# Kernel tuning notes

Measured on AMD Instinct MI355X. Metric: run time of the kernel, lower is better.

Reference implementation:

```python
import jax, jax.numpy as jnp
import numpy as np

L, B, T, E, NH, HD, HID, V = 8, 2, 2048, 1024, 16, 64, 2816, 32000


def _rmsnorm(x, w, eps=1e-6):
    return w * (x * jax.lax.rsqrt(jnp.mean(x * x, axis=-1, keepdims=True) + eps))


def _rope(x, cos, sin):
    # x: [B,H,T,D]; cos/sin: [1,1,T,D/2]
    x1, x2 = jnp.split(x, 2, axis=-1)
    return jnp.concatenate([x1 * cos - x2 * sin, x1 * sin + x2 * cos], axis=-1)


def setup_inputs() -> dict:
    key = jax.random.key(0)
    ks = jax.random.split(key, 7)
    s = 0.02
    return {
        "idx": jax.random.randint(ks[0], (B, T), 0, V),
        "tok_emb": jax.random.normal(ks[1], (V, E), dtype=jnp.float32) * s,
        "qkv_w": jax.random.normal(ks[2], (L, 3 * E, E), dtype=jnp.float32) * s,
        "proj_w": jax.random.normal(ks[3], (L, E, E), dtype=jnp.float32) * s,
        "w1": jax.random.normal(ks[4], (L, HID, E), dtype=jnp.float32) * s,
        "w2": jax.random.normal(ks[5], (L, HID, E), dtype=jnp.float32) * s,
        "w3": jax.random.normal(ks[6], (L, E, HID), dtype=jnp.float32) * s,
        "norm1_w": jnp.ones((L, E), dtype=jnp.float32),
        "norm2_w": jnp.ones((L, E), dtype=jnp.float32),
        "norm_f_w": jnp.ones((E,), dtype=jnp.float32),
    }


def reference(idx, tok_emb, qkv_w, proj_w, w1, w2, w3, norm1_w, norm2_w, norm_f_w):
    x = tok_emb[idx]  # [B,T,E]
    # RoPE cache (start_pos=0, no kv cache -> prefill path)
    half = HD // 2
    inv_freq = 1.0 / (10000.0 ** (jnp.arange(half, dtype=jnp.float32) / half))
    pos = jnp.arange(T, dtype=jnp.float32)
    freqs = pos[:, None] * inv_freq[None, :]  # [T, D/2]
    cos = jnp.cos(freqs)[None, None]
    sin = jnp.sin(freqs)[None, None]
    causal = jnp.tril(jnp.ones((T, T), dtype=bool))
    scale = 1.0 / np.sqrt(HD).astype(np.float32)

    for l in range(L):
        # attention block
        h = _rmsnorm(x, norm1_w[l])
        qkv = h @ qkv_w[l].T  # [B,T,3E]
        q, k, v = jnp.split(qkv, 3, axis=-1)
        q = q.reshape(B, T, NH, HD).transpose(0, 2, 1, 3)
        k = k.reshape(B, T, NH, HD).transpose(0, 2, 1, 3)
        v = v.reshape(B, T, NH, HD).transpose(0, 2, 1, 3)
        q = _rope(q, cos, sin)
        k = _rope(k, cos, sin)
        att = jnp.einsum('bhqd,bhkd->bhqk', q, k) * scale
        att = jnp.where(causal, att, -jnp.inf)
        att = jax.nn.softmax(att, axis=-1)
        o = jnp.einsum('bhqk,bhkd->bhqd', att, v)
        o = o.transpose(0, 2, 1, 3).reshape(B, T, E)
        x = x + o @ proj_w[l].T
        # SwiGLU MLP
        h = _rmsnorm(x, norm2_w[l])
        x = x + (jax.nn.silu(h @ w1[l].T) * (h @ w2[l].T)) @ w3[l].T

    x = _rmsnorm(x, norm_f_w)
    logits = x @ tok_emb.T  # tied lm_head
    return logits
```

## Files before the change

### kernel.cpp

```cpp
#include <hip/hip_runtime.h>

#define GLOBAL_AS __attribute__((address_space(1)))
#define LDS_AS __attribute__((address_space(3)))

typedef unsigned short u16;
typedef unsigned int u32;
typedef __attribute__((ext_vector_type(4))) float f32x4;
typedef __attribute__((ext_vector_type(8))) short bf16x8;

#define TT 2048
#define EE 1024
#define NHH 16
#define HDD 64
#define HIDD 2816
#define VV 32000
#define MM 4096

__device__ __forceinline__ u16 f2bf(float f) {
  u32 u = __builtin_bit_cast(u32, f);
  u += 0x7fffu + ((u >> 16) & 1u);
  return (u16)(u >> 16);
}
__device__ __forceinline__ float bf2f(u16 v) {
  return __builtin_bit_cast(float, (u32)v << 16);
}


__global__ __launch_bounds__(256) void castbf_k(const float* __restrict__ in,
                                                u16* __restrict__ o, long n4) {
  const long i = (long)blockIdx.x * 256 + threadIdx.x;
  if (i >= n4) return;
  const float4 v = ((const float4*)in)[i];
  ((uint2*)o)[i] = make_uint2((u32)f2bf(v.x) | ((u32)f2bf(v.y) << 16),
                              (u32)f2bf(v.z) | ((u32)f2bf(v.w) << 16));
}

__global__ void ropetab_k(float* __restrict__ cosT, float* __restrict__ sinT) {
  const int t = blockIdx.x, j = threadIdx.x;
  const float inv = powf(10000.0f, -(float)j * (1.0f / 32.0f));
  const float f = (float)t * inv;
  cosT[t * 32 + j] = cosf(f);
  sinT[t * 32 + j] = sinf(f);
}

__global__ __launch_bounds__(256) void embed_k(const int* __restrict__ idx,
                                               const float* __restrict__ temb,
                                               float* __restrict__ x) {
  const int row = blockIdx.x;
  const int id = idx[row];
  ((float4*)(x + (size_t)row * EE))[threadIdx.x] =
      ((const float4*)(temb + (size_t)id * EE))[threadIdx.x];
}

__global__ __launch_bounds__(256) void rmsnorm_k(const float* __restrict__ x,
                                                 const float* __restrict__ w,
                                                 u16* __restrict__ o) {
  __shared__ float red[4];
  const int row = blockIdx.x, tid = threadIdx.x;
  const float4 v = ((const float4*)(x + (size_t)row * EE))[tid];
  float ss = v.x * v.x + v.y * v.y + v.z * v.z + v.w * v.w;
#pragma unroll
  for (int off = 32; off; off >>= 1) ss += __shfl_xor(ss, off, 64);
  if ((tid & 63) == 0) red[tid >> 6] = ss;
  __syncthreads();
  const float inv = rsqrtf((red[0] + red[1] + red[2] + red[3]) * (1.0f / 1024.0f) + 1e-6f);
  const float4 wv = ((const float4*)w)[tid];
  const u32 lo = (u32)f2bf(v.x * inv * wv.x) | ((u32)f2bf(v.y * inv * wv.y) << 16);
  const u32 hi = (u32)f2bf(v.z * inv * wv.z) | ((u32)f2bf(v.w * inv * wv.w) << 16);
  ((uint2*)(o + (size_t)row * EE))[tid] = make_uint2(lo, hi);
}

__global__ __launch_bounds__(512) void split_rope_k(const u16* __restrict__ qkv,
                                                    const float* __restrict__ cosT,
                                                    const float* __restrict__ sinT,
                                                    u16* __restrict__ Q, u16* __restrict__ Kc,
                                                    u16* __restrict__ Vt) {
  const int row = blockIdx.x;
  const int b = row >> 11, t = row & 2047;
  const int h = threadIdx.x >> 5, j = threadIdx.x & 31;
  const u16* base = qkv + (size_t)row * (3 * EE);
  const float c = cosT[t * 32 + j], s = sinT[t * 32 + j];
  const float q1 = bf2f(base[h * 64 + j]), q2 = bf2f(base[h * 64 + j + 32]);
  const float k1 = bf2f(base[EE + h * 64 + j]), k2 = bf2f(base[EE + h * 64 + j + 32]);
  const float v1 = bf2f(base[2 * EE + h * 64 + j]), v2 = bf2f(base[2 * EE + h * 64 + j + 32]);
  const size_t bh = (size_t)(b * NHH + h);
  Q[(bh * TT + t) * HDD + j] = f2bf(q1 * c - q2 * s);
  Q[(bh * TT + t) * HDD + j + 32] = f2bf(q1 * s + q2 * c);
  Kc[(bh * TT + t) * HDD + j] = f2bf(k1 * c - k2 * s);
  Kc[(bh * TT + t) * HDD + j + 32] = f2bf(k1 * s + k2 * c);
  Vt[(bh * HDD + j) * TT + t] = f2bf(v1);
  Vt[(bh * HDD + j + 32) * TT + t] = f2bf(v2);
}

template <int OUTBF>
__global__ __launch_bounds__(512, 2) void gemm256p(const u16* __restrict__ A,
                                                   const u16* __restrict__ Bw,
                                                   float* __restrict__ C,
                                                   u16* __restrict__ C16,
                                                   const u16* __restrict__ G,
                                                   int N, int K) {
  __shared__ u16 lds[2 * 32768];
  const int t = threadIdx.x;
  const int lane = t & 63;
  const int wid = t >> 6;
  const int wr = wid >> 2;
  const int wc = wid & 3;
  const int l15 = lane & 15, lg = lane >> 4;
  const int bid = blockIdx.x;
  const int row0 = (bid & 15) << 8;
  const int col0 = (bid >> 4) << 8;
  const int NT = K >> 6;

  const int sr = t >> 3;
  const int su8 = (((t & 7) ^ (sr & 7)) << 3);
  const int t8 = t << 3;
  const u16* aG[4];
#pragma unroll
  for (int ga = 0; ga < 4; ++ga)
    aG[ga] = A + (size_t)(row0 + ga * 64 + sr) * K + su8;
  const u16* bG[4];
#pragma unroll
  for (int gb = 0; gb < 4; ++gb) {
    const int q = (gb * 2 + (sr >> 5)) & 3;
    const int nh = gb >> 1;
    bG[gb] = Bw + (size_t)(col0 + q * 64 + nh * 32 + (sr & 31)) * K + su8;
  }

  const int u0 = ((lg ^ (l15 & 7)) << 3);
  const int u1 = (((4 | lg) ^ (l15 & 7)) << 3);
  const int arow = (wr * 128 + l15) << 6;
  const int brow = 16384 + ((wc * 32 + l15) << 6);

  f32x4 acc[8][4] = {};

#define STA(nb, ga, k0n)                                                              \
  __builtin_amdgcn_global_load_lds((const GLOBAL_AS void*)(aG[ga] + (k0n)),           \
                                   (LDS_AS void*)((nb) + (ga)*4096 + t8), 16, 0, 0)
#define STB(nb, gb, k0n)                                                              \
  __builtin_amdgcn_global_load_lds((const GLOBAL_AS void*)(bG[gb] + (k0n)),           \
                                   (LDS_AS void*)((nb) + 16384 + (gb)*4096 + t8), 16, 0, 0)

  {
    u16* nb = lds;
    STA(nb, 0, 0); STA(nb, 2, 0);
    STB(nb, 0, 0); STB(nb, 1, 0);
    STB(nb, 2, 0); STB(nb, 3, 0);
    STA(nb, 1, 0); STA(nb, 3, 0);
  }

  bf16x8 af[4][2], bl[2][2], bh[2][2];

  for (int kt = 0; kt < NT; ++kt) {
    const bool st = (kt + 1 < NT);
    const int k0n = (kt + 1) << 6;
    const u16* cb = lds + (kt & 1) * 32768;
    u16* nb = lds + ((kt + 1) & 1) * 32768;

    asm volatile("s_waitcnt vmcnt(4)" ::: "memory");
    __builtin_amdgcn_s_barrier();
#pragma unroll
    for (int mi = 0; mi < 4; ++mi) {
      af[mi][0] = *(const bf16x8*)&cb[arow + mi * 1024 + u0];
      af[mi][1] = *(const bf16x8*)&cb[arow + mi * 1024 + u1];
    }
#pragma unroll
    for (int ni = 0; ni < 2; ++ni) {
      bl[ni][0] = *(const bf16x8*)&cb[brow + ni * 1024 + u0];
      bl[ni][1] = *(const bf16x8*)&cb[brow + ni * 1024 + u1];
    }
    if (st) { STA(nb, 0, k0n); STA(nb, 2, k0n); }
    __builtin_amdgcn_s_setprio(1);
#pragma unroll
    for (int mi = 0; mi < 4; ++mi)
#pragma unroll
      for (int ni = 0; ni < 2; ++ni) {
        acc[mi][ni] = __builtin_amdgcn_mfma_f32_16x16x32_bf16(af[mi][0], bl[ni][0], acc[mi][ni], 0, 0, 0);
        acc[mi][ni] = __builtin_amdgcn_mfma_f32_16x16x32_bf16(af[mi][1], bl[ni][1], acc[mi][ni], 0, 0, 0);
      }
    __builtin_amdgcn_s_setprio(0);

    if (st) { asm volatile("s_waitcnt vmcnt(4)" ::: "memory"); }
    else    { asm volatile("s_waitcnt vmcnt(2)" ::: "memory"); }
    __builtin_amdgcn_s_barrier();
#pragma unroll
    for (int ni = 0; ni < 2; ++ni) {
      bh[ni][0] = *(const bf16x8*)&cb[brow + 8192 + ni * 1024 + u0];
      bh[ni][1] = *(const bf16x8*)&cb[brow + 8192 + ni * 1024 + u1];
    }
    if (st) { STB(nb, 0, k0n); STB(nb, 1, k0n); }
    __builtin_amdgcn_s_setprio(1);
#pragma unroll
    for (int mi = 0; mi < 4; ++mi)
#pragma unroll
      for (int ni = 0; ni < 2; ++ni) {
        acc[mi][2 + ni] = __builtin_amdgcn_mfma_f32_16x16x32_bf16(af[mi][0], bh[ni][0], acc[mi][2 + ni], 0, 0, 0);
        acc[mi][2 + ni] = __builtin_amdgcn_mfma_f32_16x16x32_bf16(af[mi][1], bh[ni][1], acc[mi][2 + ni], 0, 0, 0);
      }
    __builtin_amdgcn_s_setprio(0);

    if (st) { asm volatile("s_waitcnt vmcnt(4)" ::: "memory"); }
    else    { asm volatile("s_waitcnt vmcnt(0)" ::: "memory"); }
    __builtin_amdgcn_s_barrier();
#pragma unroll
    for (int mi = 0; mi < 4; ++mi) {
      af[mi][0] = *(const bf16x8*)&cb[arow + (4 + mi) * 1024 + u0];
      af[mi][1] = *(const bf16x8*)&cb[arow + (4 + mi) * 1024 + u1];
    }
    if (st) { STB(nb, 2, k0n); STB(nb, 3, k0n); }
    __builtin_amdgcn_s_setprio(1);
#pragma unroll
    for (int mi = 0; mi < 4; ++mi)
#pragma unroll
      for (int ni = 0; ni < 2; ++ni) {
        acc[4 + mi][2 + ni] = __builtin_amdgcn_mfma_f32_16x16x32_bf16(af[mi][0], bh[ni][0], acc[4 + mi][2 + ni], 0, 0, 0);
        acc[4 + mi][2 + ni] = __builtin_amdgcn_mfma_f32_16x16x32_bf16(af[mi][1], bh[ni][1], acc[4 + mi][2 + ni], 0, 0, 0);
      }
    __builtin_amdgcn_s_setprio(0);

    if (st) { STA(nb, 1, k0n); STA(nb, 3, k0n); }
    __builtin_amdgcn_s_setprio(1);
#pragma unroll
    for (int mi = 0; mi < 4; ++mi)
#pragma unroll
      for (int ni = 0; ni < 2; ++ni) {
        acc[4 + mi][ni] = __builtin_amdgcn_mfma_f32_16x16x32_bf16(af[mi][0], bl[ni][0], acc[4 + mi][ni], 0, 0, 0);
        acc[4 + mi][ni] = __builtin_amdgcn_mfma_f32_16x16x32_bf16(af[mi][1], bl[ni][1], acc[4 + mi][ni], 0, 0, 0);
      }
    __builtin_amdgcn_s_setprio(0);
  }
#undef STA
#undef STB

#pragma unroll
  for (int m = 0; m < 8; ++m) {
    const int row = row0 + wr * 128 + m * 16 + lg * 4;
#pragma unroll
    for (int n = 0; n < 4; ++n) {
      const int col = col0 + wc * 64 + n * 16 + l15;
#pragma unroll
      for (int r = 0; r < 4; ++r) {
        const size_t o = (size_t)(row + r) * N + col;
        if (OUTBF == 0) {
          C[o] = acc[m][n][r];
        } else if (OUTBF == 1) {
          C16[o] = f2bf(acc[m][n][r]);
        } else {
          const float g = bf2f(G[o]);
          C16[o] = f2bf(g / (1.0f + __expf(-g)) * acc[m][n][r]);
        }
      }
    }
  }
}

__global__ __launch_bounds__(256, 2) void gemm128r(const u16* __restrict__ A,
                                                   const u16* __restrict__ Bw,
                                                   float* __restrict__ C,
                                                   const float* __restrict__ R,
                                                   int N, int K) {
  __shared__ u16 lds[4 * 8192];
  const int t = threadIdx.x;
  const int lane = t & 63;
  const int wid = t >> 6;
  const int wr = wid >> 1;
  const int wc = wid & 1;
  const int l15 = lane & 15, lg = lane >> 4;
  const int bid = blockIdx.x;
  const int row0 = (bid & 31) << 7;
  const int col0 = (bid >> 5) << 7;
  const int NT = K >> 5;

  const int rA = t >> 2;
  const int usw = (((t & 3) ^ ((t >> 3) & 3)) << 3);
  const u16* sA0 = A + (size_t)(row0 + rA) * K + usw;
  const u16* sA1 = A + (size_t)(row0 + 64 + rA) * K + usw;
  const u16* sB0 = Bw + (size_t)(col0 + rA) * K + usw;
  const u16* sB1 = Bw + (size_t)(col0 + 64 + rA) * K + usw;
  const int dst = t << 3;

  const int e8 = ((lg ^ ((l15 >> 1) & 3)) << 3);
  const int aoff = (wr * 64 + l15) * 32 + e8;
  const int boff = 4096 + (wc * 64 + l15) * 32 + e8;

  f32x4 acc[4][4] = {};

  auto stage = [&](int kt) {
    u16* base = &lds[(kt & 3) * 8192];
    const size_t ko = (size_t)kt * 32;
    __builtin_amdgcn_global_load_lds((const GLOBAL_AS void*)(sA0 + ko),
                                     (LDS_AS void*)(base + dst), 16, 0, 0);
    __builtin_amdgcn_global_load_lds((const GLOBAL_AS void*)(sA1 + ko),
                                     (LDS_AS void*)(base + 2048 + dst), 16, 0, 0);
    __builtin_amdgcn_global_load_lds((const GLOBAL_AS void*)(sB0 + ko),
                                     (LDS_AS void*)(base + 4096 + dst), 16, 0, 0);
    __builtin_amdgcn_global_load_lds((const GLOBAL_AS void*)(sB1 + ko),
                                     (LDS_AS void*)(base + 6144 + dst), 16, 0, 0);
  };

  stage(0);
  stage(1);
  stage(2);

  for (int kt = 0; kt < NT; ++kt) {
    const int rem = NT - 1 - kt;
    if (rem >= 2) {
      asm volatile("s_waitcnt vmcnt(8)" ::: "memory");
    } else if (rem == 1) {
      asm volatile("s_waitcnt vmcnt(4)" ::: "memory");
    } else {
      asm volatile("s_waitcnt vmcnt(0)" ::: "memory");
    }
    __builtin_amdgcn_s_barrier();
    if (kt + 3 < NT) stage(kt + 3);
    const u16* base = &lds[(kt & 3) * 8192];
    bf16x8 af[4], bfv[4];
#pragma unroll
    for (int m = 0; m < 4; ++m) af[m] = *(const bf16x8*)&base[aoff + m * 512];
#pragma unroll
    for (int n = 0; n < 4; ++n) bfv[n] = *(const bf16x8*)&base[boff + n * 512];
    __builtin_amdgcn_s_setprio(1);
#pragma unroll
    for (int m = 0; m < 4; ++m)
#pragma unroll
      for (int n = 0; n < 4; ++n)
        acc[m][n] = __builtin_amdgcn_mfma_f32_16x16x32_bf16(af[m], bfv[n], acc[m][n], 0, 0, 0);
    __builtin_amdgcn_s_setprio(0);
  }

#pragma unroll
  for (int m = 0; m < 4; ++m) {
    const int row = row0 + wr * 64 + m * 16 + lg * 4;
#pragma unroll
    for (int n = 0; n < 4; ++n) {
      const int col = col0 + wc * 64 + n * 16 + l15;
#pragma unroll
      for (int r = 0; r < 4; ++r) {
        const size_t o = (size_t)(row + r) * N + col;
        C[o] = acc[m][n][r] + R[o];
      }
    }
  }
}

__global__ __launch_bounds__(256) void attn_k(const u16* __restrict__ Q,
                                              const u16* __restrict__ Kc,
                                              const u16* __restrict__ Vt,
                                              u16* __restrict__ O) {
  __shared__ u16 P_lds[4][32][72];
  const int bh = blockIdx.y;
  const int q0 = blockIdx.x * 128;
  const int lane = threadIdx.x & 63;
  const int w = threadIdx.x >> 6;
  const int l15 = lane & 15, lg = lane >> 4;
  const int qbase = q0 + w * 32;

  bf16x8 qf[2][2];
#pragma unroll
  for (int am = 0; am < 2; ++am)
#pragma unroll
    for (int ks = 0; ks < 2; ++ks)
      qf[am][ks] = *(const bf16x8*)&Q[((size_t)bh * TT + qbase + am * 16 + l15) * HDD + ks * 32 + lg * 8];

  bf16x8 ones;
#pragma unroll
  for (int i = 0; i < 8; ++i) ones[i] = (short)0x3F80;

  f32x4 oacc[2][4] = {};
  f32x4 lacc[2] = {};

  const int ntile = (q0 + 128) >> 6;
  for (int kt = 0; kt < ntile; ++kt) {
    const int k0 = kt << 6;
    f32x4 s[2][4];
    bf16x8 kf0[4], kf1[4];
#pragma unroll
    for (int an = 0; an < 4; ++an) {
      kf0[an] = *(const bf16x8*)&Kc[((size_t)bh * TT + k0 + an * 16 + l15) * HDD + lg * 8];
      kf1[an] = *(const bf16x8*)&Kc[((size_t)bh * TT + k0 + an * 16 + l15) * HDD + 32 + lg * 8];
    }
    __builtin_amdgcn_s_setprio(1);
#pragma unroll
    for (int an = 0; an < 4; ++an) {
#pragma unroll
      for (int am = 0; am < 2; ++am) {
        f32x4 z = {0.0f, 0.0f, 0.0f, 0.0f};
        z = __builtin_amdgcn_mfma_f32_16x16x32_bf16(qf[am][0], kf0[an], z, 0, 0, 0);
        s[am][an] = __builtin_amdgcn_mfma_f32_16x16x32_bf16(qf[am][1], kf1[an], z, 0, 0, 0);
      }
    }
    __builtin_amdgcn_s_setprio(0);
    const bool diag = (k0 + 64) > q0;
#pragma unroll
    for (int am = 0; am < 2; ++am)
#pragma unroll
      for (int an = 0; an < 4; ++an)
#pragma unroll
        for (int r = 0; r < 4; ++r) {
          float v = s[am][an][r] * 0.125f;
          if (diag) {
            const int qrow = qbase + am * 16 + lg * 4 + r;
            const int kcol = k0 + an * 16 + l15;
            if (kcol > qrow) v = -1e30f;
          }
          s[am][an][r] = __expf(v);
        }
#pragma unroll
    for (int am = 0; am < 2; ++am)
#pragma unroll
      for (int an = 0; an < 4; ++an)
#pragma unroll
        for (int r = 0; r < 4; ++r)
          P_lds[w][am * 16 + lg * 4 + r][an * 16 + l15] = f2bf(s[am][an][r]);
#pragma unroll
    for (int ks = 0; ks < 2; ++ks) {
      bf16x8 pf[2];
#pragma unroll
      for (int am = 0; am < 2; ++am)
        pf[am] = *(const bf16x8*)&P_lds[w][am * 16 + l15][ks * 32 + lg * 8];
      __builtin_amdgcn_s_setprio(1);
#pragma unroll
      for (int dn = 0; dn < 4; ++dn) {
        const bf16x8 vf = *(const bf16x8*)&Vt[((size_t)bh * HDD + dn * 16 + l15) * TT + k0 + ks * 32 + lg * 8];
#pragma unroll
        for (int am = 0; am < 2; ++am)
          oacc[am][dn] = __builtin_amdgcn_mfma_f32_16x16x32_bf16(pf[am], vf, oacc[am][dn], 0, 0, 0);
      }
#pragma unroll
      for (int am = 0; am < 2; ++am)
        lacc[am] = __builtin_amdgcn_mfma_f32_16x16x32_bf16(pf[am], ones, lacc[am], 0, 0, 0);
      __builtin_amdgcn_s_setprio(0);
    }
  }
  const int b = bh >> 4, h = bh & 15;
#pragma unroll
  for (int am = 0; am < 2; ++am)
#pragma unroll
    for (int r = 0; r < 4; ++r) {
      const float il = 1.0f / lacc[am][r];
      const int qrow = qbase + am * 16 + lg * 4 + r;
#pragma unroll
      for (int dn = 0; dn < 4; ++dn)
        O[((size_t)b * TT + qrow) * EE + h * 64 + dn * 16 + l15] = f2bf(oacc[am][dn][r] * il);
    }
}


extern "C" void kernel_launch(void* const* d_in, const int* in_sizes, int n_in,
                              void* d_out, int out_size, void* d_ws, size_t ws_size,
                              hipStream_t stream) {
  const int* idx = (const int*)d_in[0];
  const float* tok_emb = (const float*)d_in[1];
  const float* qkv_w = (const float*)d_in[2];
  const float* proj_w = (const float*)d_in[3];
  const float* w1 = (const float*)d_in[4];
  const float* w2 = (const float*)d_in[5];
  const float* w3 = (const float*)d_in[6];
  const float* norm1_w = (const float*)d_in[7];
  const float* norm2_w = (const float*)d_in[8];
  const float* norm_f_w = (const float*)d_in[9];
  float* out = (float*)d_out;

  char* ws = (char*)d_ws;
  size_t off = 0;
  auto alloc = [&](size_t bytes) -> void* {
    off = (off + 255) & ~(size_t)255;
    void* p = ws + off;
    off += bytes;
    return p;
  };

  const size_t N_TEMB = (size_t)VV * EE;
  const size_t N_QKVW = (size_t)8 * 3 * EE * EE;
  const size_t N_PROJW = (size_t)8 * EE * EE;
  const size_t N_W1 = (size_t)8 * HIDD * EE;
  const size_t N_W3 = (size_t)8 * EE * HIDD;

  u16* tembbf = (u16*)alloc(N_TEMB * 2);
  u16* qkvwbf = (u16*)alloc(N_QKVW * 2);
  u16* projwbf = (u16*)alloc(N_PROJW * 2);
  u16* w1bf = (u16*)alloc(N_W1 * 2);
  u16* w2bf = (u16*)alloc(N_W1 * 2);
  u16* w3bf = (u16*)alloc(N_W3 * 2);
  float* x = (float*)alloc((size_t)MM * EE * 4);
  u16* h1 = (u16*)alloc((size_t)MM * EE * 2);
  u16* hg = (u16*)alloc((size_t)MM * HIDD * 2);
  u16* qb = (u16*)alloc((size_t)2 * NHH * TT * HDD * 2);
  u16* kb = (u16*)alloc((size_t)2 * NHH * TT * HDD * 2);
  u16* vtb = (u16*)alloc((size_t)2 * NHH * TT * HDD * 2);
  u16* attno = (u16*)alloc((size_t)MM * EE * 2);
  float* cosT = (float*)alloc((size_t)TT * 32 * 4);
  float* sinT = (float*)alloc((size_t)TT * 32 * 4);

  u16* qkv16 = (u16*)out;
  u16* g16 = (u16*)(out + 16777216);

  auto cast = [&](const float* src, u16* dst, size_t n) {
    const long n4 = (long)(n / 4);
    castbf_k<<<(int)((n4 + 255) / 256), 256, 0, stream>>>(src, dst, n4);
  };
  cast(tok_emb, tembbf, N_TEMB);
  cast(qkv_w, qkvwbf, N_QKVW);
  cast(proj_w, projwbf, N_PROJW);
  cast(w1, w1bf, N_W1);
  cast(w2, w2bf, N_W1);
  cast(w3, w3bf, N_W3);

  ropetab_k<<<TT, 32, 0, stream>>>(cosT, sinT);
  embed_k<<<MM, 256, 0, stream>>>(idx, tok_emb, x);

  for (int l = 0; l < 8; ++l) {
    rmsnorm_k<<<MM, 256, 0, stream>>>(x, norm1_w + l * EE, h1);
    gemm256p<1><<<dim3(12 * 16), 512, 0, stream>>>(h1, qkvwbf + (size_t)l * 3 * EE * EE,
                                                   nullptr, qkv16, nullptr, 3 * EE, EE);
    split_rope_k<<<MM, 512, 0, stream>>>(qkv16, cosT, sinT, qb, kb, vtb);
    attn_k<<<dim3(16, 32), 256, 0, stream>>>(qb, kb, vtb, attno);
    gemm128r<<<dim3(8 * 32), 256, 0, stream>>>(attno, projwbf + (size_t)l * EE * EE,
                                               x, x, EE, EE);
    rmsnorm_k<<<MM, 256, 0, stream>>>(x, norm2_w + l * EE, h1);
    gemm256p<1><<<dim3(11 * 16), 512, 0, stream>>>(h1, w1bf + (size_t)l * HIDD * EE,
                                                   nullptr, g16, nullptr, HIDD, EE);
    gemm256p<2><<<dim3(11 * 16), 512, 0, stream>>>(h1, w2bf + (size_t)l * HIDD * EE,
                                                   nullptr, hg, g16, HIDD, EE);
    gemm128r<<<dim3(8 * 32), 256, 0, stream>>>(hg, w3bf + (size_t)l * EE * HIDD,
                                               x, x, EE, HIDD);
  }
  rmsnorm_k<<<MM, 256, 0, stream>>>(x, norm_f_w, h1);
  gemm256p<0><<<dim3(125 * 16), 512, 0, stream>>>(h1, tembbf, out, nullptr, nullptr, VV, EE);
}
```

Measured before the change: 2.962 ms.

## Fuse RoPE and Q/K/V head split into QKV GEMM epilogue

Removes the separate split_rope kernel and the bf16 QKV intermediate buffer. The QKV GEMM now applies RoPE and writes Q, K and transposed V directly from its accumulators in a new epilogue mode. It also changes the B-tile LDS layout to contiguous 64-row groups, which pairs dims j and j+32 inside one wave. The main loop gets a different prefetch order, wait counts and extra barriers. This saves a launch and a round trip of the QKV activations, in exchange for a scattered epilogue store pattern and more barriers in every GEMM.

```diff
diff --git a/kernel.cpp b/kernel.cpp
--- a/kernel.cpp
+++ b/kernel.cpp
@@ -70,34 +70,17 @@
   ((uint2*)(o + (size_t)row * EE))[tid] = make_uint2(lo, hi);
 }
 
-__global__ __launch_bounds__(512) void split_rope_k(const u16* __restrict__ qkv,
-                                                    const float* __restrict__ cosT,
-                                                    const float* __restrict__ sinT,
-                                                    u16* __restrict__ Q, u16* __restrict__ Kc,
-                                                    u16* __restrict__ Vt) {
-  const int row = blockIdx.x;
-  const int b = row >> 11, t = row & 2047;
-  const int h = threadIdx.x >> 5, j = threadIdx.x & 31;
-  const u16* base = qkv + (size_t)row * (3 * EE);
-  const float c = cosT[t * 32 + j], s = sinT[t * 32 + j];
-  const float q1 = bf2f(base[h * 64 + j]), q2 = bf2f(base[h * 64 + j + 32]);
-  const float k1 = bf2f(base[EE + h * 64 + j]), k2 = bf2f(base[EE + h * 64 + j + 32]);
-  const float v1 = bf2f(base[2 * EE + h * 64 + j]), v2 = bf2f(base[2 * EE + h * 64 + j + 32]);
-  const size_t bh = (size_t)(b * NHH + h);
-  Q[(bh * TT + t) * HDD + j] = f2bf(q1 * c - q2 * s);
-  Q[(bh * TT + t) * HDD + j + 32] = f2bf(q1 * s + q2 * c);
-  Kc[(bh * TT + t) * HDD + j] = f2bf(k1 * c - k2 * s);
-  Kc[(bh * TT + t) * HDD + j + 32] = f2bf(k1 * s + k2 * c);
-  Vt[(bh * HDD + j) * TT + t] = f2bf(v1);
-  Vt[(bh * HDD + j + 32) * TT + t] = f2bf(v2);
-}
-
 template <int OUTBF>
 __global__ __launch_bounds__(512, 2) void gemm256p(const u16* __restrict__ A,
                                                    const u16* __restrict__ Bw,
                                                    float* __restrict__ C,
                                                    u16* __restrict__ C16,
                                                    const u16* __restrict__ G,
+                                                   const float* __restrict__ cosT,
+                                                   const float* __restrict__ sinT,
+                                                   u16* __restrict__ Qb,
+                                                   u16* __restrict__ Kb,
+                                                   u16* __restrict__ Vtb,
                                                    int N, int K) {
   __shared__ u16 lds[2 * 32768];
   const int t = threadIdx.x;
@@ -115,121 +98,159 @@
   const int su8 = (((t & 7) ^ (sr & 7)) << 3);
   const int t8 = t << 3;
   const u16* aG[4];
-#pragma unroll
-  for (int ga = 0; ga < 4; ++ga)
-    aG[ga] = A + (size_t)(row0 + ga * 64 + sr) * K + su8;
   const u16* bG[4];
 #pragma unroll
-  for (int gb = 0; gb < 4; ++gb) {
-    const int q = (gb * 2 + (sr >> 5)) & 3;
-    const int nh = gb >> 1;
-    bG[gb] = Bw + (size_t)(col0 + q * 64 + nh * 32 + (sr & 31)) * K + su8;
-  }
-
-  const int u0 = ((lg ^ (l15 & 7)) << 3);
-  const int u1 = (((4 | lg) ^ (l15 & 7)) << 3);
-  const int arow = (wr * 128 + l15) << 6;
-  const int brow = 16384 + ((wc * 32 + l15) << 6);
+  for (int g = 0; g < 4; ++g) {
+    aG[g] = A + (size_t)(row0 + g * 64 + sr) * K + su8;
+    bG[g] = Bw + (size_t)(col0 + g * 64 + sr) * K + su8;
+  }
+
+  const int swz = l15 & 7;
+  const int u0 = ((lg ^ swz) << 3);
+  const int u1 = (((4 | lg) ^ swz) << 3);
+  const int abase = (wr * 2) * 4096 + l15 * 64;
+  const int bbase = 16384 + wc * 4096 + l15 * 64;
 
   f32x4 acc[8][4] = {};
 
-#define STA(nb, ga, k0n)                                                              \
-  __builtin_amdgcn_global_load_lds((const GLOBAL_AS void*)(aG[ga] + (k0n)),           \
+#define STA(nb, ga, ko)                                                               \
+  __builtin_amdgcn_global_load_lds((const GLOBAL_AS void*)(aG[ga] + (ko)),            \
                                    (LDS_AS void*)((nb) + (ga)*4096 + t8), 16, 0, 0)
-#define STB(nb, gb, k0n)                                                              \
-  __builtin_amdgcn_global_load_lds((const GLOBAL_AS void*)(bG[gb] + (k0n)),           \
+#define STB(nb, gb, ko)                                                               \
+  __builtin_amdgcn_global_load_lds((const GLOBAL_AS void*)(bG[gb] + (ko)),            \
                                    (LDS_AS void*)((nb) + 16384 + (gb)*4096 + t8), 16, 0, 0)
 
   {
     u16* nb = lds;
-    STA(nb, 0, 0); STA(nb, 2, 0);
-    STB(nb, 0, 0); STB(nb, 1, 0);
-    STB(nb, 2, 0); STB(nb, 3, 0);
+    STA(nb, 0, 0); STA(nb, 2, 0); STB(nb, 0, 0);
+    STB(nb, 1, 0); STB(nb, 2, 0); STB(nb, 3, 0);
     STA(nb, 1, 0); STA(nb, 3, 0);
   }
-
-  bf16x8 af[4][2], bl[2][2], bh[2][2];
 
   for (int kt = 0; kt < NT; ++kt) {
     const bool st = (kt + 1 < NT);
-    const int k0n = (kt + 1) << 6;
+    const int ko = (kt + 1) << 6;
     const u16* cb = lds + (kt & 1) * 32768;
     u16* nb = lds + ((kt + 1) & 1) * 32768;
-
-    asm volatile("s_waitcnt vmcnt(4)" ::: "memory");
+    bf16x8 a0[4][2], a1[4][2], b0[2][2], b1[2][2];
+
+    asm volatile("s_waitcnt vmcnt(2)" ::: "memory");
     __builtin_amdgcn_s_barrier();
 #pragma unroll
     for (int mi = 0; mi < 4; ++mi) {
-      af[mi][0] = *(const bf16x8*)&cb[arow + mi * 1024 + u0];
-      af[mi][1] = *(const bf16x8*)&cb[arow + mi * 1024 + u1];
+      a0[mi][0] = *(const bf16x8*)&cb[abase + mi * 1024 + u0];
+      a0[mi][1] = *(const bf16x8*)&cb[abase + mi * 1024 + u1];
     }
 #pragma unroll
     for (int ni = 0; ni < 2; ++ni) {
-      bl[ni][0] = *(const bf16x8*)&cb[brow + ni * 1024 + u0];
-      bl[ni][1] = *(const bf16x8*)&cb[brow + ni * 1024 + u1];
-    }
-    if (st) { STA(nb, 0, k0n); STA(nb, 2, k0n); }
+      b0[ni][0] = *(const bf16x8*)&cb[bbase + ni * 1024 + u0];
+      b0[ni][1] = *(const bf16x8*)&cb[bbase + ni * 1024 + u1];
+    }
+    if (st) { STA(nb, 0, ko); STA(nb, 2, ko); STB(nb, 0, ko); }
+    __builtin_amdgcn_s_barrier();
     __builtin_amdgcn_s_setprio(1);
 #pragma unroll
     for (int mi = 0; mi < 4; ++mi)
 #pragma unroll
       for (int ni = 0; ni < 2; ++ni) {
-        acc[mi][ni] = __builtin_amdgcn_mfma_f32_16x16x32_bf16(af[mi][0], bl[ni][0], acc[mi][ni], 0, 0, 0);
-        acc[mi][ni] = __builtin_amdgcn_mfma_f32_16x16x32_bf16(af[mi][1], bl[ni][1], acc[mi][ni], 0, 0, 0);
+        acc[mi][ni] = __builtin_amdgcn_mfma_f32_16x16x32_bf16(a0[mi][0], b0[ni][0], acc[mi][ni], 0, 0, 0);
+        acc[mi][ni] = __builtin_amdgcn_mfma_f32_16x16x32_bf16(a0[mi][1], b0[ni][1], acc[mi][ni], 0, 0, 0);
       }
     __builtin_amdgcn_s_setprio(0);
-
-    if (st) { asm volatile("s_waitcnt vmcnt(4)" ::: "memory"); }
-    else    { asm volatile("s_waitcnt vmcnt(2)" ::: "memory"); }
-    __builtin_amdgcn_s_barrier();
+    __builtin_amdgcn_s_barrier();
+
 #pragma unroll
     for (int ni = 0; ni < 2; ++ni) {
-      bh[ni][0] = *(const bf16x8*)&cb[brow + 8192 + ni * 1024 + u0];
-      bh[ni][1] = *(const bf16x8*)&cb[brow + 8192 + ni * 1024 + u1];
-    }
-    if (st) { STB(nb, 0, k0n); STB(nb, 1, k0n); }
+      b1[ni][0] = *(const bf16x8*)&cb[bbase + (2 + ni) * 1024 + u0];
+      b1[ni][1] = *(const bf16x8*)&cb[bbase + (2 + ni) * 1024 + u1];
+    }
+    if (st) {
+      STB(nb, 1, ko); STB(nb, 2, ko); STB(nb, 3, ko);
+      asm volatile("s_waitcnt vmcnt(6)" ::: "memory");
+    } else {
+      asm volatile("s_waitcnt vmcnt(0)" ::: "memory");
+    }
+    __builtin_amdgcn_s_barrier();
+#pragma unroll
+    for (int mi = 0; mi < 4; ++mi) {
+      a1[mi][0] = *(const bf16x8*)&cb[abase + 4096 + mi * 1024 + u0];
+      a1[mi][1] = *(const bf16x8*)&cb[abase + 4096 + mi * 1024 + u1];
+    }
     __builtin_amdgcn_s_setprio(1);
 #pragma unroll
     for (int mi = 0; mi < 4; ++mi)
 #pragma unroll
       for (int ni = 0; ni < 2; ++ni) {
-        acc[mi][2 + ni] = __builtin_amdgcn_mfma_f32_16x16x32_bf16(af[mi][0], bh[ni][0], acc[mi][2 + ni], 0, 0, 0);
-        acc[mi][2 + ni] = __builtin_amdgcn_mfma_f32_16x16x32_bf16(af[mi][1], bh[ni][1], acc[mi][2 + ni], 0, 0, 0);
+        acc[mi][2 + ni] = __builtin_amdgcn_mfma_f32_16x16x32_bf16(a0[mi][0], b1[ni][0], acc[mi][2 + ni], 0, 0, 0);
+        acc[mi][2 + ni] = __builtin_amdgcn_mfma_f32_16x16x32_bf16(a0[mi][1], b1[ni][1], acc[mi][2 + ni], 0, 0, 0);
       }
     __builtin_amdgcn_s_setprio(0);
-
-    if (st) { asm volatile("s_waitcnt vmcnt(4)" ::: "memory"); }
-    else    { asm volatile("s_waitcnt vmcnt(0)" ::: "memory"); }
-    __builtin_amdgcn_s_barrier();
-#pragma unroll
-    for (int mi = 0; mi < 4; ++mi) {
-      af[mi][0] = *(const bf16x8*)&cb[arow + (4 + mi) * 1024 + u0];
-      af[mi][1] = *(const bf16x8*)&cb[arow + (4 + mi) * 1024 + u1];
-    }
-    if (st) { STB(nb, 2, k0n); STB(nb, 3, k0n); }
+    __builtin_amdgcn_s_barrier();
+
+    if (st) { STA(nb, 1, ko); STA(nb, 3, ko); }
     __builtin_amdgcn_s_setprio(1);
 #pragma unroll
     for (int mi = 0; mi < 4; ++mi)
 #pragma unroll
       for (int ni = 0; ni < 2; ++ni) {
-        acc[4 + mi][2 + ni] = __builtin_amdgcn_mfma_f32_16x16x32_bf16(af[mi][0], bh[ni][0], acc[4 + mi][2 + ni], 0, 0, 0);
-        acc[4 + mi][2 + ni] = __builtin_amdgcn_mfma_f32_16x16x32_bf16(af[mi][1], bh[ni][1], acc[4 + mi][2 + ni], 0, 0, 0);
+        acc[4 + mi][2 + ni] = __builtin_amdgcn_mfma_f32_16x16x32_bf16(a1[mi][0], b1[ni][0], acc[4 + mi][2 + ni], 0, 0, 0);
+        acc[4 + mi][2 + ni] = __builtin_amdgcn_mfma_f32_16x16x32_bf16(a1[mi][1], b1[ni][1], acc[4 + mi][2 + ni], 0, 0, 0);
       }
     __builtin_amdgcn_s_setprio(0);
-
-    if (st) { STA(nb, 1, k0n); STA(nb, 3, k0n); }
+    __builtin_amdgcn_s_barrier();
+
     __builtin_amdgcn_s_setprio(1);
 #pragma unroll
     for (int mi = 0; mi < 4; ++mi)
 #pragma unroll
       for (int ni = 0; ni < 2; ++ni) {
-        acc[4 + mi][ni] = __builtin_amdgcn_mfma_f32_16x16x32_bf16(af[mi][0], bl[ni][0], acc[4 + mi][ni], 0, 0, 0);
-        acc[4 + mi][ni] = __builtin_amdgcn_mfma_f32_16x16x32_bf16(af[mi][1], bl[ni][1], acc[4 + mi][ni], 0, 0, 0);
+        acc[4 + mi][ni] = __builtin_amdgcn_mfma_f32_16x16x32_bf16(a1[mi][0], b0[ni][0], acc[4 + mi][ni], 0, 0, 0);
+        acc[4 + mi][ni] = __builtin_amdgcn_mfma_f32_16x16x32_bf16(a1[mi][1], b0[ni][1], acc[4 + mi][ni], 0, 0, 0);
       }
     __builtin_amdgcn_s_setprio(0);
   }
 #undef STA
 #undef STB
+
+  if (OUTBF == 3) {
+    const int reg = col0 >> 10;
+    const int fb = col0 & 1023;
+#pragma unroll
+    for (int m = 0; m < 8; ++m) {
+      const int row = row0 + wr * 128 + m * 16 + lg * 4;
+      const int b = row >> 11, tbase = row & 2047;
+      if (reg < 2) {
+        u16* dst = (reg == 0) ? Qb : Kb;
+#pragma unroll
+        for (int n = 0; n < 2; ++n) {
+          const int f = fb + wc * 64 + n * 16 + l15;
+          const int h = f >> 6, j = f & 63;
+#pragma unroll
+          for (int r = 0; r < 4; ++r) {
+            const int tt = tbase + r;
+            const float c = cosT[tt * 32 + j], s = sinT[tt * 32 + j];
+            const float x1 = acc[m][n][r], x2 = acc[m][n | 2][r];
+            const size_t ro = ((size_t)(b * NHH + h) * TT + tt) * HDD + j;
+            dst[ro] = f2bf(x1 * c - x2 * s);
+            dst[ro + 32] = f2bf(x1 * s + x2 * c);
+          }
+        }
+      } else {
+#pragma unroll
+        for (int n = 0; n < 4; ++n) {
+          const int f = fb + wc * 64 + n * 16 + l15;
+          const int h = f >> 6, j = f & 63;
+          ushort4 pk;
+          pk.x = f2bf(acc[m][n][0]);
+          pk.y = f2bf(acc[m][n][1]);
+          pk.z = f2bf(acc[m][n][2]);
+          pk.w = f2bf(acc[m][n][3]);
+          *(ushort4*)&Vtb[((size_t)(b * NHH + h) * HDD + j) * TT + tbase] = pk;
+        }
+      }
+    }
+    return;
+  }
 
 #pragma unroll
   for (int m = 0; m < 8; ++m) {
@@ -491,7 +512,6 @@
   float* cosT = (float*)alloc((size_t)TT * 32 * 4);
   float* sinT = (float*)alloc((size_t)TT * 32 * 4);
 
-  u16* qkv16 = (u16*)out;
   u16* g16 = (u16*)(out + 16777216);
 
   auto cast = [&](const float* src, u16* dst, size_t n) {
@@ -510,20 +530,26 @@
 
   for (int l = 0; l < 8; ++l) {
     rmsnorm_k<<<MM, 256, 0, stream>>>(x, norm1_w + l * EE, h1);
-    gemm256p<1><<<dim3(12 * 16), 512, 0, stream>>>(h1, qkvwbf + (size_t)l * 3 * EE * EE,
-                                                   nullptr, qkv16, nullptr, 3 * EE, EE);
-    split_rope_k<<<MM, 512, 0, stream>>>(qkv16, cosT, sinT, qb, kb, vtb);
+    gemm256p<3><<<dim3(12 * 16), 512, 0, stream>>>(h1, qkvwbf + (size_t)l * 3 * EE * EE,
+                                                   nullptr, nullptr, nullptr,
+                                                   cosT, sinT, qb, kb, vtb, 3 * EE, EE);
     attn_k<<<dim3(16, 32), 256, 0, stream>>>(qb, kb, vtb, attno);
     gemm128r<<<dim3(8 * 32), 256, 0, stream>>>(attno, projwbf + (size_t)l * EE * EE,
                                                x, x, EE, EE);
     rmsnorm_k<<<MM, 256, 0, stream>>>(x, norm2_w + l * EE, h1);
     gemm256p<1><<<dim3(11 * 16), 512, 0, stream>>>(h1, w1bf + (size_t)l * HIDD * EE,
-                                                   nullptr, g16, nullptr, HIDD, EE);
+                                                   nullptr, g16, nullptr,
+                                                   nullptr, nullptr, nullptr, nullptr, nullptr,
+                                                   HIDD, EE);
     gemm256p<2><<<dim3(11 * 16), 512, 0, stream>>>(h1, w2bf + (size_t)l * HIDD * EE,
-                                                   nullptr, hg, g16, HIDD, EE);
+                                                   nullptr, hg, g16,
+                                                   nullptr, nullptr, nullptr, nullptr, nullptr,
+                                                   HIDD, EE);
     gemm128r<<<dim3(8 * 32), 256, 0, stream>>>(hg, w3bf + (size_t)l * EE * HIDD,
                                                x, x, EE, HIDD);
   }
   rmsnorm_k<<<MM, 256, 0, stream>>>(x, norm_f_w, h1);
-  gemm256p<0><<<dim3(125 * 16), 512, 0, stream>>>(h1, tembbf, out, nullptr, nullptr, VV, EE);
-}
+  gemm256p<0><<<dim3(125 * 16), 512, 0, stream>>>(h1, tembbf, out, nullptr, nullptr,
+                                                  nullptr, nullptr, nullptr, nullptr, nullptr,
+                                                  VV, EE);
+}
```

New measurement: 2.830 ms. -4.5%, faster.

## Fuse RoPE and QKV split into QKV GEMM epilogue; widen residual GEMM to 512 threads

Applied to the files above, without the earlier changes.

Adds a QKV GEMM epilogue that applies RoPE, folds the attention scale into Q, and writes Q, K and transposed V directly, removing the split_rope kernel and the bf16 qkv round trip through memory. The attention kernel no longer multiplies scores by the scale. The residual GEMM now runs 8 waves per block with a 32-column slice per wave and one A/B load per thread per stage, with wait counts adjusted to match. The epilogue does scattered 2-byte stores and per-element cos/sin loads, and the new wave split changes occupancy and LDS reuse.

```diff
diff --git a/kernel.cpp b/kernel.cpp
--- a/kernel.cpp
+++ b/kernel.cpp
@@ -70,34 +70,17 @@
   ((uint2*)(o + (size_t)row * EE))[tid] = make_uint2(lo, hi);
 }
 
-__global__ __launch_bounds__(512) void split_rope_k(const u16* __restrict__ qkv,
-                                                    const float* __restrict__ cosT,
-                                                    const float* __restrict__ sinT,
-                                                    u16* __restrict__ Q, u16* __restrict__ Kc,
-                                                    u16* __restrict__ Vt) {
-  const int row = blockIdx.x;
-  const int b = row >> 11, t = row & 2047;
-  const int h = threadIdx.x >> 5, j = threadIdx.x & 31;
-  const u16* base = qkv + (size_t)row * (3 * EE);
-  const float c = cosT[t * 32 + j], s = sinT[t * 32 + j];
-  const float q1 = bf2f(base[h * 64 + j]), q2 = bf2f(base[h * 64 + j + 32]);
-  const float k1 = bf2f(base[EE + h * 64 + j]), k2 = bf2f(base[EE + h * 64 + j + 32]);
-  const float v1 = bf2f(base[2 * EE + h * 64 + j]), v2 = bf2f(base[2 * EE + h * 64 + j + 32]);
-  const size_t bh = (size_t)(b * NHH + h);
-  Q[(bh * TT + t) * HDD + j] = f2bf(q1 * c - q2 * s);
-  Q[(bh * TT + t) * HDD + j + 32] = f2bf(q1 * s + q2 * c);
-  Kc[(bh * TT + t) * HDD + j] = f2bf(k1 * c - k2 * s);
-  Kc[(bh * TT + t) * HDD + j + 32] = f2bf(k1 * s + k2 * c);
-  Vt[(bh * HDD + j) * TT + t] = f2bf(v1);
-  Vt[(bh * HDD + j + 32) * TT + t] = f2bf(v2);
-}
-
 template <int OUTBF>
 __global__ __launch_bounds__(512, 2) void gemm256p(const u16* __restrict__ A,
                                                    const u16* __restrict__ Bw,
                                                    float* __restrict__ C,
                                                    u16* __restrict__ C16,
                                                    const u16* __restrict__ G,
+                                                   const float* __restrict__ cosT,
+                                                   const float* __restrict__ sinT,
+                                                   u16* __restrict__ Qb,
+                                                   u16* __restrict__ Kb,
+                                                   u16* __restrict__ Vtb,
                                                    int N, int K) {
   __shared__ u16 lds[2 * 32768];
   const int t = threadIdx.x;
@@ -231,6 +214,47 @@
 #undef STA
 #undef STB
 
+  if (OUTBF == 3) {
+    const int reg = col0 >> 10;
+    const int fb = col0 & 1023;
+#pragma unroll
+    for (int m = 0; m < 8; ++m) {
+      const int row = row0 + wr * 128 + m * 16 + lg * 4;
+      const int b = row >> 11, tbase = row & 2047;
+      if (reg < 2) {
+        u16* dstp = (reg == 0) ? Qb : Kb;
+        const float qs = (reg == 0) ? 0.125f : 1.0f;
+#pragma unroll
+        for (int n = 0; n < 2; ++n) {
+          const int f = fb + wc * 64 + n * 16 + l15;
+          const int h = f >> 6, j = f & 63;
+#pragma unroll
+          for (int r = 0; r < 4; ++r) {
+            const int tt = tbase + r;
+            const float c = cosT[tt * 32 + j], s = sinT[tt * 32 + j];
+            const float x1 = acc[m][n][r], x2 = acc[m][n | 2][r];
+            const size_t ro = ((size_t)(b * NHH + h) * TT + tt) * HDD + j;
+            dstp[ro] = f2bf((x1 * c - x2 * s) * qs);
+            dstp[ro + 32] = f2bf((x1 * s + x2 * c) * qs);
+          }
+        }
+      } else {
+#pragma unroll
+        for (int n = 0; n < 4; ++n) {
+          const int f = fb + wc * 64 + n * 16 + l15;
+          const int h = f >> 6, j = f & 63;
+          ushort4 pk;
+          pk.x = f2bf(acc[m][n][0]);
+          pk.y = f2bf(acc[m][n][1]);
+          pk.z = f2bf(acc[m][n][2]);
+          pk.w = f2bf(acc[m][n][3]);
+          *(ushort4*)&Vtb[((size_t)(b * NHH + h) * HDD + j) * TT + tbase] = pk;
+        }
+      }
+    }
+    return;
+  }
+
 #pragma unroll
   for (int m = 0; m < 8; ++m) {
     const int row = row0 + wr * 128 + m * 16 + lg * 4;
@@ -253,7 +277,7 @@
   }
 }
 
-__global__ __launch_bounds__(256, 2) void gemm128r(const u16* __restrict__ A,
+__global__ __launch_bounds__(512, 2) void gemm128r(const u16* __restrict__ A,
                                                    const u16* __restrict__ Bw,
                                                    float* __restrict__ C,
                                                    const float* __restrict__ R,
@@ -262,8 +286,8 @@
   const int t = threadIdx.x;
   const int lane = t & 63;
   const int wid = t >> 6;
-  const int wr = wid >> 1;
-  const int wc = wid & 1;
+  const int wr = wid >> 2;
+  const int wc = wid & 3;
   const int l15 = lane & 15, lg = lane >> 4;
   const int bid = blockIdx.x;
   const int row0 = (bid & 31) << 7;
@@ -272,29 +296,23 @@
 
   const int rA = t >> 2;
   const int usw = (((t & 3) ^ ((t >> 3) & 3)) << 3);
-  const u16* sA0 = A + (size_t)(row0 + rA) * K + usw;
-  const u16* sA1 = A + (size_t)(row0 + 64 + rA) * K + usw;
-  const u16* sB0 = Bw + (size_t)(col0 + rA) * K + usw;
-  const u16* sB1 = Bw + (size_t)(col0 + 64 + rA) * K + usw;
+  const u16* sA = A + (size_t)(row0 + rA) * K + usw;
+  const u16* sB = Bw + (size_t)(col0 + rA) * K + usw;
   const int dst = t << 3;
 
   const int e8 = ((lg ^ ((l15 >> 1) & 3)) << 3);
   const int aoff = (wr * 64 + l15) * 32 + e8;
-  const int boff = 4096 + (wc * 64 + l15) * 32 + e8;
-
-  f32x4 acc[4][4] = {};
+  const int boff = 4096 + (wc * 32 + l15) * 32 + e8;
+
+  f32x4 acc[4][2] = {};
 
   auto stage = [&](int kt) {
     u16* base = &lds[(kt & 3) * 8192];
     const size_t ko = (size_t)kt * 32;
-    __builtin_amdgcn_global_load_lds((const GLOBAL_AS void*)(sA0 + ko),
+    __builtin_amdgcn_global_load_lds((const GLOBAL_AS void*)(sA + ko),
                                      (LDS_AS void*)(base + dst), 16, 0, 0);
-    __builtin_amdgcn_global_load_lds((const GLOBAL_AS void*)(sA1 + ko),
-                                     (LDS_AS void*)(base + 2048 + dst), 16, 0, 0);
-    __builtin_amdgcn_global_load_lds((const GLOBAL_AS void*)(sB0 + ko),
+    __builtin_amdgcn_global_load_lds((const GLOBAL_AS void*)(sB + ko),
                                      (LDS_AS void*)(base + 4096 + dst), 16, 0, 0);
-    __builtin_amdgcn_global_load_lds((const GLOBAL_AS void*)(sB1 + ko),
-                                     (LDS_AS void*)(base + 6144 + dst), 16, 0, 0);
   };
 
   stage(0);
@@ -304,25 +322,25 @@
   for (int kt = 0; kt < NT; ++kt) {
     const int rem = NT - 1 - kt;
     if (rem >= 2) {
-      asm volatile("s_waitcnt vmcnt(8)" ::: "memory");
+      asm volatile("s_waitcnt vmcnt(4)" ::: "memory");
     } else if (rem == 1) {
-      asm volatile("s_waitcnt vmcnt(4)" ::: "memory");
+      asm volatile("s_waitcnt vmcnt(2)" ::: "memory");
     } else {
       asm volatile("s_waitcnt vmcnt(0)" ::: "memory");
     }
     __builtin_amdgcn_s_barrier();
     if (kt + 3 < NT) stage(kt + 3);
     const u16* base = &lds[(kt & 3) * 8192];
-    bf16x8 af[4], bfv[4];
+    bf16x8 af[4], bfv[2];
 #pragma unroll
     for (int m = 0; m < 4; ++m) af[m] = *(const bf16x8*)&base[aoff + m * 512];
 #pragma unroll
-    for (int n = 0; n < 4; ++n) bfv[n] = *(const bf16x8*)&base[boff + n * 512];
+    for (int n = 0; n < 2; ++n) bfv[n] = *(const bf16x8*)&base[boff + n * 512];
     __builtin_amdgcn_s_setprio(1);
 #pragma unroll
     for (int m = 0; m < 4; ++m)
 #pragma unroll
-      for (int n = 0; n < 4; ++n)
+      for (int n = 0; n < 2; ++n)
         acc[m][n] = __builtin_amdgcn_mfma_f32_16x16x32_bf16(af[m], bfv[n], acc[m][n], 0, 0, 0);
     __builtin_amdgcn_s_setprio(0);
   }
@@ -331,8 +349,8 @@
   for (int m = 0; m < 4; ++m) {
     const int row = row0 + wr * 64 + m * 16 + lg * 4;
 #pragma unroll
-    for (int n = 0; n < 4; ++n) {
-      const int col = col0 + wc * 64 + n * 16 + l15;
+    for (int n = 0; n < 2; ++n) {
+      const int col = col0 + wc * 32 + n * 16 + l15;
 #pragma unroll
       for (int r = 0; r < 4; ++r) {
         const size_t o = (size_t)(row + r) * N + col;
@@ -396,7 +414,7 @@
       for (int an = 0; an < 4; ++an)
 #pragma unroll
         for (int r = 0; r < 4; ++r) {
-          float v = s[am][an][r] * 0.125f;
+          float v = s[am][an][r];
           if (diag) {
             const int qrow = qbase + am * 16 + lg * 4 + r;
             const int kcol = k0 + an * 16 + l15;
@@ -491,7 +509,6 @@
   float* cosT = (float*)alloc((size_t)TT * 32 * 4);
   float* sinT = (float*)alloc((size_t)TT * 32 * 4);
 
-  u16* qkv16 = (u16*)out;
   u16* g16 = (u16*)(out + 16777216);
 
   auto cast = [&](const float* src, u16* dst, size_t n) {
@@ -510,20 +527,26 @@
 
   for (int l = 0; l < 8; ++l) {
     rmsnorm_k<<<MM, 256, 0, stream>>>(x, norm1_w + l * EE, h1);
-    gemm256p<1><<<dim3(12 * 16), 512, 0, stream>>>(h1, qkvwbf + (size_t)l * 3 * EE * EE,
-                                                   nullptr, qkv16, nullptr, 3 * EE, EE);
-    split_rope_k<<<MM, 512, 0, stream>>>(qkv16, cosT, sinT, qb, kb, vtb);
+    gemm256p<3><<<dim3(12 * 16), 512, 0, stream>>>(h1, qkvwbf + (size_t)l * 3 * EE * EE,
+                                                   nullptr, nullptr, nullptr,
+                                                   cosT, sinT, qb, kb, vtb, 3 * EE, EE);
     attn_k<<<dim3(16, 32), 256, 0, stream>>>(qb, kb, vtb, attno);
-    gemm128r<<<dim3(8 * 32), 256, 0, stream>>>(attno, projwbf + (size_t)l * EE * EE,
+    gemm128r<<<dim3(8 * 32), 512, 0, stream>>>(attno, projwbf + (size_t)l * EE * EE,
                                                x, x, EE, EE);
     rmsnorm_k<<<MM, 256, 0, stream>>>(x, norm2_w + l * EE, h1);
     gemm256p<1><<<dim3(11 * 16), 512, 0, stream>>>(h1, w1bf + (size_t)l * HIDD * EE,
-                                                   nullptr, g16, nullptr, HIDD, EE);
+                                                   nullptr, g16, nullptr,
+                                                   nullptr, nullptr, nullptr, nullptr, nullptr,
+                                                   HIDD, EE);
     gemm256p<2><<<dim3(11 * 16), 512, 0, stream>>>(h1, w2bf + (size_t)l * HIDD * EE,
-                                                   nullptr, hg, g16, HIDD, EE);
-    gemm128r<<<dim3(8 * 32), 256, 0, stream>>>(hg, w3bf + (size_t)l * EE * HIDD,
+                                                   nullptr, hg, g16,
+                                                   nullptr, nullptr, nullptr, nullptr, nullptr,
+                                                   HIDD, EE);
+    gemm128r<<<dim3(8 * 32), 512, 0, stream>>>(hg, w3bf + (size_t)l * EE * HIDD,
                                                x, x, EE, HIDD);
   }
   rmsnorm_k<<<MM, 256, 0, stream>>>(x, norm_f_w, h1);
-  gemm256p<0><<<dim3(125 * 16), 512, 0, stream>>>(h1, tembbf, out, nullptr, nullptr, VV, EE);
-}
+  gemm256p<0><<<dim3(125 * 16), 512, 0, stream>>>(h1, tembbf, out, nullptr, nullptr,
+                                                  nullptr, nullptr, nullptr, nullptr, nullptr,
+                                                  VV, EE);
+}
```

Result: faster. 2.741 ms (-7.5%).
